# Kernel optimization log

Hardware: AMD Instinct MI355X
Metric: run time of the kernel (lower is better)

The kernel has to match this reference:

```python
import jax, jax.numpy as jnp
import numpy as np
import math

B, S, H, NH = 4, 1024, 1536, 24
DH = H // NH
BUCKETS = 256          # position_buckets
MAX_REL = 512          # max_relative_positions
ATT_SPAN = BUCKETS     # pos_ebd_size
SCALE_FACTOR = 3       # 1 (content) + c2p + p2c
LN_EPS = 1e-7


def _make_log_bucket(rel, bucket_size, max_position):
    # numpy port of make_log_bucket_position (used only to build inputs)
    sign = np.sign(rel)
    mid = bucket_size // 2
    abs_pos = np.where((rel < mid) & (rel > -mid), mid - 1, np.abs(rel)).astype(np.float64)
    log_pos = np.ceil(np.log(abs_pos / mid) / np.log((max_position - 1) / mid) * (mid - 1)) + mid
    bucket = np.where(abs_pos <= mid, rel.astype(np.float64), log_pos * sign)
    return bucket.astype(np.int64)


def setup_inputs() -> dict:
    key = jax.random.key(0)
    ks = jax.random.split(key, 8)
    s = 0.02
    hidden_states = jax.random.normal(ks[0], (B, S, H), jnp.float32)
    rel_embeddings = jax.random.normal(ks[1], (2 * ATT_SPAN, H), jnp.float32)
    ids = np.arange(S)
    relative_pos = jnp.asarray(
        _make_log_bucket(ids[:, None] - ids[None, :], BUCKETS, MAX_REL)[None].astype(np.int32))  # [1,S,S]
    lengths = np.full((B,), S)
    lengths[B // 2:] = (3 * S) // 4  # some padded sequences
    valid = np.arange(S)[None, :] < lengths[:, None]  # [B,S]
    attention_mask = jnp.asarray(
        (valid[:, None, :, None] & valid[:, None, None, :]).astype(np.int32))  # [B,1,S,S]
    Wq = jax.random.normal(ks[2], (H, H), jnp.float32) * s
    Wk = jax.random.normal(ks[3], (H, H), jnp.float32) * s
    Wv = jax.random.normal(ks[4], (H, H), jnp.float32) * s
    Wo = jax.random.normal(ks[5], (H, H), jnp.float32) * s
    z = jnp.zeros((H,), jnp.float32)
    return dict(hidden_states=hidden_states, rel_embeddings=rel_embeddings,
                Wq=Wq, bq=z, Wk=Wk, bk=z, Wv=Wv, bv=z, Wo=Wo, bo=z,
                ln_g=jnp.ones((H,), jnp.float32), ln_b=z,
                attention_mask=attention_mask, relative_pos=relative_pos)


def _attention(hidden_states, rel_embeddings, Wq, bq, Wk, bk, Wv, bv, Wo, bo,
               ln_g, ln_b, attention_mask, relative_pos):
    Bm, Sm, Hm = hidden_states.shape

    def heads(x):  # [B,S,H] -> [B,NH,S,DH]
        return x.reshape(Bm, Sm, NH, DH).transpose(0, 2, 1, 3)

    q = heads(hidden_states @ Wq + bq)
    k = heads(hidden_states @ Wk + bk)
    v = heads(hidden_states @ Wv + bv)

    scale = math.sqrt(DH * SCALE_FACTOR)
    scores = jnp.einsum('bhqd,bhkd->bhqk', q, k) / scale  # content-to-content

    # share_att_key=True: reuse query/key projections on rel embeddings
    pos_k = (rel_embeddings @ Wk + bk).reshape(2 * ATT_SPAN, NH, DH).transpose(1, 0, 2)  # [NH,2P,DH]
    pos_q = (rel_embeddings @ Wq + bq).reshape(2 * ATT_SPAN, NH, DH).transpose(1, 0, 2)

    # content -> position
    c2p = jnp.einsum('bhqd,hpd->bhqp', q, pos_k)  # [B,NH,S,2P]
    c2p_idx = jnp.clip(relative_pos + ATT_SPAN, 0, 2 * ATT_SPAN - 1)[:, None]  # [1,1,S,S]
    c2p = jnp.take_along_axis(c2p, jnp.broadcast_to(c2p_idx, (Bm, NH, Sm, Sm)), axis=-1)
    scores = scores + c2p / scale

    # position -> content
    p2c = jnp.einsum('bhkd,hpd->bhkp', k, pos_q)  # [B,NH,S,2P]
    p2c_idx = jnp.clip(-relative_pos + ATT_SPAN, 0, 2 * ATT_SPAN - 1)[:, None]
    p2c = jnp.take_along_axis(p2c, jnp.broadcast_to(p2c_idx, (Bm, NH, Sm, Sm)), axis=-1)
    scores = scores + jnp.swapaxes(p2c, -1, -2) / scale

    # XSoftmax: mask==0 -> -inf before softmax, 0 after
    m = attention_mask.astype(bool)
    neg = jnp.finfo(scores.dtype).min
    probs = jax.nn.softmax(jnp.where(m, scores, neg), axis=-1)
    probs = jnp.where(m, probs, jnp.zeros((), scores.dtype))

    ctx = jnp.einsum('bhqk,bhkd->bhqd', probs, v)
    ctx = ctx.transpose(0, 2, 1, 3).reshape(Bm, Sm, Hm)

    # DebertaV2SelfOutput: dense + residual + LayerNorm
    out = ctx @ Wo + bo + hidden_states
    mu = jnp.mean(out, axis=-1, keepdims=True)
    var = jnp.mean(jnp.square(out - mu), axis=-1, keepdims=True)
    return (out - mu) / jnp.sqrt(var + LN_EPS) * ln_g + ln_b


def reference(hidden_states, rel_embeddings, Wq, bq, Wk, bk, Wv, bv, Wo, bo,
              ln_g, ln_b, attention_mask, relative_pos):
    return _attention(hidden_states, rel_embeddings, Wq, bq, Wk, bk, Wv, bv,
                      Wo, bo, ln_g, ln_b, attention_mask, relative_pos)
```

## Files before the change

### kernel.cpp

```cpp
#include <hip/hip_runtime.h>
#include <hip/hip_bf16.h>

constexpr int Bc  = 4;
constexpr int Sc  = 1024;
constexpr int Hc  = 1536;
constexpr int NHc = 24;
constexpr int P2c = 512;
constexpr int MX  = Bc * Sc;
constexpr int MA  = MX + P2c;
constexpr int N3  = 3 * Hc;
constexpr float INV_SCALE = 0.07216878364870323f;

using f32x4  = __attribute__((ext_vector_type(4))) float;
using bf16x8 = __attribute__((ext_vector_type(8))) short;
using i32x4  = __attribute__((ext_vector_type(4))) int;
using u16x8  = __attribute__((ext_vector_type(8))) unsigned short;
using u16x4  = __attribute__((ext_vector_type(4))) unsigned short;
typedef unsigned short u16;
typedef unsigned int u32;

#define DEV __device__ __forceinline__

DEV float bf2f(u16 u) { return __uint_as_float(((unsigned)u) << 16); }
DEV u16   f2bf(float f) { return __builtin_bit_cast(unsigned short, __float2bfloat16(f)); }

#if defined(__has_builtin)
#if __has_builtin(__builtin_amdgcn_global_load_lds)
#define HAVE_GLL 1
#endif
#endif
#ifndef HAVE_GLL
#define HAVE_GLL 0
#endif

DEV void stage32(u16* lds, const u16* g, int ldk, int lane) {
#pragma unroll
  for (int c = 0; c < 4; ++c) {
    const int row   = c * 8 + (lane >> 3);
    const int gslot = (lane & 7) ^ (row & 7);
    const u16* gp = g + (size_t)row * ldk + gslot * 8;
#if HAVE_GLL
    __builtin_amdgcn_global_load_lds(
        (const __attribute__((address_space(1))) void*)gp,
        (__attribute__((address_space(3))) void*)(lds + c * 8 * 64),
        16, 0, 0);
#else
    i32x4 v = *(const i32x4*)gp;
    *(i32x4*)(lds + row * 64 + (lane & 7) * 8) = v;
#endif
  }
}

DEV bf16x8 ldsFrag(const u16* base, int row, int kh, int lhi) {
  const int idx = row * 64 + ((kh * 32 + lhi * 8) ^ ((row & 7) * 8));
  return *(const bf16x8*)(base + idx);
}

template <int MODE>
__global__ __launch_bounds__(256) void gemm128(
    const u16* __restrict__ A, const u16* __restrict__ Bt,
    const float* __restrict__ bias, const float* __restrict__ resid,
    u16* __restrict__ outb, float* __restrict__ outf, u16* __restrict__ vtout, int ldo)
{
  __shared__ alignas(16) u16 As[128 * 64];
  __shared__ alignas(16) u16 Bs[128 * 64];
  const int tid = threadIdx.x, wid = tid >> 6, lane = tid & 63;
  const int wr = wid >> 1, wc = wid & 1;
  const int l15 = lane & 15, lhi = lane >> 4;
  int bx, by;
  if (MODE == 0) {
    int id = blockIdx.x;
    id = (id & 7) * 138 + (id >> 3);
    if (id < 1008) {
      const int q = id / 36;
      by = q < 22 ? q : q + 2;
      bx = id - q * 36;
    } else {
      const int r = id - 1008;
      by = 32 + r / 24;
      bx = r % 24;
    }
  } else { bx = blockIdx.x; by = blockIdx.y; }
  const int m0 = by * 128, n0 = bx * 128;

  f32x4 acc[4][4] = {};
#pragma unroll 1
  for (int kt = 0; kt < 24; ++kt) {
    const int k0 = kt * 64;
    stage32(As + wid * (32 * 64), A  + (size_t)(m0 + wid * 32) * 1536 + k0, 1536, lane);
    stage32(Bs + wid * (32 * 64), Bt + (size_t)(n0 + wid * 32) * 1536 + k0, 1536, lane);
    asm volatile("s_waitcnt vmcnt(0)" ::: "memory");
    __syncthreads();
#pragma unroll
    for (int kh = 0; kh < 2; ++kh) {
      bf16x8 af[4], bfv[4];
#pragma unroll
      for (int mt = 0; mt < 4; ++mt) af[mt]  = ldsFrag(As, wr * 64 + mt * 16 + l15, kh, lhi);
#pragma unroll
      for (int nt = 0; nt < 4; ++nt) bfv[nt] = ldsFrag(Bs, wc * 64 + nt * 16 + l15, kh, lhi);
#pragma unroll
      for (int mt = 0; mt < 4; ++mt)
#pragma unroll
        for (int nt = 0; nt < 4; ++nt)
          acc[mt][nt] = __builtin_amdgcn_mfma_f32_16x16x32_bf16(af[mt], bfv[nt], acc[mt][nt], 0, 0, 0);
    }
    __syncthreads();
  }
#pragma unroll
  for (int mt = 0; mt < 4; ++mt)
#pragma unroll
    for (int nt = 0; nt < 4; ++nt) {
      const int gn = n0 + wc * 64 + nt * 16 + l15;
      const float bs = bias[gn];
      if (MODE == 0) {
        u16x4 q4;
#pragma unroll
        for (int r = 0; r < 4; ++r) {
          const int gm = m0 + wr * 64 + mt * 16 + lhi * 4 + r;
          float v = acc[mt][nt][r] + bs;
          if (gn < Hc) v *= INV_SCALE;
          q4[r] = f2bf(v);
          outb[(size_t)gm * ldo + gn] = q4[r];
        }
        if (gn >= 2 * Hc && m0 < MX) {
          const int b = m0 >> 10;
          const int krow = (m0 & 1023) + wr * 64 + mt * 16 + (lhi << 2);
          *(u16x4*)(vtout + ((size_t)(b * 1536 + (gn - 2 * Hc))) * Sc + krow) = q4;
        }
      } else {
#pragma unroll
        for (int r = 0; r < 4; ++r) {
          const int gm = m0 + wr * 64 + mt * 16 + lhi * 4 + r;
          outf[(size_t)gm * ldo + gn] = acc[mt][nt][r] + bs + resid[(size_t)gm * ldo + gn];
        }
      }
    }
}

__global__ __launch_bounds__(256) void prep2(
    const float* __restrict__ bq, const float* __restrict__ bk, const float* __restrict__ bv,
    const int* __restrict__ am, const int* __restrict__ rp,
    float* __restrict__ bias, u32* __restrict__ TBL2, int* __restrict__ LENS)
{
  const int TOT = N3 + 2048;
  for (int i = blockIdx.x * 256 + threadIdx.x; i < TOT; i += gridDim.x * 256) {
    if (i < N3) {
      bias[i] = i < Hc ? bq[i] : (i < 2 * Hc ? bk[i - Hc] : bv[i - 2 * Hc]);
    } else {
      const int t = i - N3;
      auto Tf = [&](int tt) -> u32 {
        tt = tt > 2046 ? 2046 : tt;
        const int d = tt - 1023;
        int v = (d >= 0 ? rp[(size_t)d * Sc] : rp[-d]) + 256;
        return (u32)(v < 0 ? 0 : (v > 511 ? 511 : v));
      };
      TBL2[t] = Tf(t) | (Tf(t + 1) << 16);
    }
  }
  if (blockIdx.x == 0) {
    const int wid = threadIdx.x >> 6, lane = threadIdx.x & 63;
    if (wid < 4) {
      int s = 0;
#pragma unroll
      for (int j = 0; j < 16; ++j) {
        const int ss = j * 64 + lane;
        s += am[(size_t)wid * Sc * Sc + (size_t)ss * Sc + ss] != 0;
      }
#pragma unroll
      for (int off = 1; off <= 32; off <<= 1) s += __shfl_xor(s, off);
      if (lane == 0) LENS[wid] = s;
    }
  }
}

__global__ __launch_bounds__(256) void cast_x(const float* __restrict__ hs,
                                              const float* __restrict__ rel,
                                              u16* __restrict__ A)
{
  const size_t total = (size_t)MA * Hc / 4;
  for (size_t i = (size_t)blockIdx.x * 256 + threadIdx.x; i < total; i += (size_t)gridDim.x * 256) {
    const size_t e = i * 4;
    const int row = (int)(e / Hc), col = (int)(e % Hc);
    const float* s = row < MX ? hs + (size_t)row * Hc + col : rel + (size_t)(row - MX) * Hc + col;
    f32x4 v = *(const f32x4*)s;
    u16x4 o = { f2bf(v[0]), f2bf(v[1]), f2bf(v[2]), f2bf(v[3]) };
    *(u16x4*)(A + e) = o;
  }
}

__global__ void transpose_cast(const float* __restrict__ Wq, const float* __restrict__ Wk,
                               const float* __restrict__ Wv, const float* __restrict__ Wo,
                               u16* __restrict__ WT, u16* __restrict__ WOT)
{
  const int z = blockIdx.z;
  const float* src = z == 0 ? Wq : z == 1 ? Wk : z == 2 ? Wv : Wo;
  u16* dst = z == 3 ? WOT : WT + (size_t)z * Hc * Hc;
  __shared__ float t[32][33];
  const int tx = threadIdx.x, ty = threadIdx.y;
  const int kb = blockIdx.y * 32, nb = blockIdx.x * 32;
#pragma unroll
  for (int i = 0; i < 4; ++i)
    t[ty + i * 8][tx] = src[(size_t)(kb + ty + i * 8) * Hc + nb + tx];
  __syncthreads();
#pragma unroll
  for (int i = 0; i < 4; ++i)
    dst[(size_t)(nb + ty + i * 8) * Hc + kb + tx] = f2bf(t[tx][ty + i * 8]);
}

__global__ __launch_bounds__(256) void relmat5(const u16* __restrict__ QKVP,
    u16* __restrict__ c2p, u16* __restrict__ p2cT, const int* __restrict__ LENS, int bh_base)
{
  const int lbh = blockIdx.x / 12, vv = blockIdx.x % 12;
  const int bh = bh_base + lbh, b = bh / NHc, h = bh % NHc;
  const int tid = threadIdx.x, wid = tid >> 6, lane = tid & 63;
  const int l15 = lane & 15, lhi = lane >> 4, lhi4 = lhi * 4;

  __shared__ alignas(16) u16 Bs[512 * 64];

  int m0, n0, ldo, nsw, brows;
  size_t arow, brow;
  u16* out;
  if (vv < 4) {
    m0 = vv * 256; n0 = 0; ldo = P2c; nsw = 32; brows = 512;
    if (m0 >= LENS[b]) return;
    arow = (size_t)b * Sc + m0; brow = (size_t)MX;
    out = c2p + (size_t)lbh * Sc * P2c;
  } else {
    const int w = vv - 4;
    m0 = (w >> 2) * 256; n0 = (w & 3) * 256; ldo = Sc; nsw = 16; brows = 256;
    if (n0 >= LENS[b]) return;
    arow = (size_t)MX + m0; brow = (size_t)b * Sc + n0;
    out = p2cT + (size_t)lbh * P2c * Sc;
  }
  const int acol = h * 64;
  const int bcol = Hc + h * 64;

  const int srow = tid >> 3;
  const int gsl  = (tid & 7) ^ (srow & 7);
  const int its = brows >> 5;
  for (int it = 0; it < its; ++it) {
    const int row = it * 32 + srow;
    const u16* gp = QKVP + (brow + row) * 4608 + bcol + gsl * 8;
#if HAVE_GLL
    __builtin_amdgcn_global_load_lds(
        (const __attribute__((address_space(1))) void*)gp,
        (__attribute__((address_space(3))) void*)(&Bs[it * 2048 + wid * 512]),
        16, 0, 0);
#else
    *(i32x4*)(&Bs[row * 64 + (tid & 7) * 8]) = *(const i32x4*)gp;
#endif
  }

  bf16x8 af[4][2];
#pragma unroll
  for (int mt = 0; mt < 4; ++mt)
#pragma unroll
    for (int kh = 0; kh < 2; ++kh)
      af[mt][kh] = *(const bf16x8*)(QKVP + (arow + wid * 64 + mt * 16 + l15) * 4608
                                    + acol + kh * 32 + lhi * 8);

  asm volatile("s_waitcnt vmcnt(0)" ::: "memory");
  __syncthreads();

#pragma unroll 4
  for (int nt = 0; nt < nsw; ++nt) {
    bf16x8 b0 = ldsFrag(Bs, nt * 16 + l15, 0, lhi);
    bf16x8 b1 = ldsFrag(Bs, nt * 16 + l15, 1, lhi);
    f32x4 acc[4] = {};
#pragma unroll
    for (int mt = 0; mt < 4; ++mt) {
      acc[mt] = __builtin_amdgcn_mfma_f32_16x16x32_bf16(af[mt][0], b0, acc[mt], 0, 0, 0);
      acc[mt] = __builtin_amdgcn_mfma_f32_16x16x32_bf16(af[mt][1], b1, acc[mt], 0, 0, 0);
    }
#pragma unroll
    for (int mt = 0; mt < 4; ++mt)
#pragma unroll
      for (int r = 0; r < 4; ++r) {
        const int mm = m0 + wid * 64 + mt * 16 + lhi4 + r;
        const int nn = n0 + nt * 16 + l15;
        out[(size_t)mm * ldo + nn] = f2bf(acc[mt][r]);
      }
  }
}

__global__ __launch_bounds__(256) void flash11(
    const u16* __restrict__ QKVP, const u16* __restrict__ VT,
    const u16* __restrict__ c2p, const u16* __restrict__ p2cT,
    const int* __restrict__ LENS, const u32* __restrict__ TBL2g,
    u16* __restrict__ ctx, int bh_base, int chunkC)
{
  int id = blockIdx.x;
  const int grid = chunkC * 16;
  if ((grid & 7) == 0) { const int cpx = grid >> 3; id = (id & 7) * cpx + (id >> 3); }
  const int lbh = id >> 4, qi = id & 15;
  const int bh = bh_base + lbh, b = bh / NHc, h = bh % NHc;
  const int q0 = qi * 64;
  const int tid = threadIdx.x, wid = tid >> 6, lane = tid & 63;
  const int l15 = lane & 15, lhi = lane >> 4, lhi4 = lhi * 4;
  const int len = LENS[b];

  if (q0 >= len) {
    u16x8 z = {};
#pragma unroll
    for (int i = 0; i < 2; ++i) {
      const int t = i * 256 + tid;
      *(u16x8*)(ctx + (size_t)(b * Sc + q0 + (t >> 3)) * Hc + h * 64 + (t & 7) * 8) = z;
    }
    return;
  }
  const int nkt = (len + 63) >> 6;
  const int qg = q0 + wid * 16 + l15;

  __shared__ u32 Lt2[2048];
  __shared__ alignas(16) u16 cWs[64 * 152];
  __shared__ alignas(16) u16 pWs[136 * 72];
  __shared__ alignas(16) u16 Kt[64 * 64];
  __shared__ alignas(16) u16 Vt[64 * 64];
  __shared__ alignas(16) u16 Pl[4][16 * 64];

  const u16* c2pB  = c2p  + (size_t)lbh * Sc * P2c;
  const u16* p2cTB = p2cT + (size_t)lbh * P2c * Sc;
  const u16* Qg  = QKVP + (size_t)b * Sc * 4608 + h * 64;
  const u16* Kg  = QKVP + (size_t)b * Sc * 4608 + Hc + h * 64;
  const u16* VTg = VT + (size_t)bh * 64 * Sc;

  for (int i = tid; i < 2048; i += 256) Lt2[i] = TBL2g[i];

  bf16x8 aq[2];
#pragma unroll
  for (int kh = 0; kh < 2; ++kh)
    aq[kh] = *(const bf16x8*)(Qg + (size_t)qg * 4608 + kh * 32 + lhi * 8);

  const int kr = tid >> 2, dc = (tid & 3) * 16;
  const int sk = (kr & 7) * 8;

  u16x8 rcw[5], rpw[5], rk0, rk1, rv0, rv1;

  auto issue = [&](int k0, int c0a) {
#pragma unroll
    for (int i = 0; i < 5; ++i) {
      const int s = i * 256 + tid;
      if (s < 1152) {
        const int row = s / 18, ch = s - row * 18;
        rcw[i] = *(const u16x8*)(c2pB + (size_t)(q0 + row) * P2c + c0a + ch * 8);
      }
    }
#pragma unroll
    for (int i = 0; i < 5; ++i) {
      const int s = i * 256 + tid;
      if (s < 1088) {
        const int row = s >> 3, ch = s & 7;
        rpw[i] = *(const u16x8*)(p2cTB + (size_t)(c0a + row) * Sc + k0 + ch * 8);
      }
    }
    const size_t ro = (size_t)(k0 + kr) * 4608 + dc;
    rk0 = *(const u16x8*)(Kg + ro); rk1 = *(const u16x8*)(Kg + ro + 8);
    const u16* vp = VTg + (size_t)kr * Sc + k0 + dc;
    rv0 = *(const u16x8*)vp; rv1 = *(const u16x8*)(vp + 8);
  };

  auto commit = [&]() {
#pragma unroll
    for (int i = 0; i < 5; ++i) {
      const int s = i * 256 + tid;
      if (s < 1152) {
        const int row = s / 18, ch = s - row * 18;
        *(u16x8*)(cWs + row * 152 + ch * 8) = rcw[i];
      }
    }
#pragma unroll
    for (int i = 0; i < 5; ++i) {
      const int s = i * 256 + tid;
      if (s < 1088) {
        const int row = s >> 3, ch = s & 7;
        *(u16x8*)(pWs + row * 72 + ch * 8) = rpw[i];
      }
    }
    *(u16x8*)(Kt + kr * 64 + (dc ^ sk))       = rk0;
    *(u16x8*)(Kt + kr * 64 + ((dc ^ sk) ^ 8)) = rk1;
    *(u16x8*)(Vt + kr * 64 + (dc ^ sk))       = rv0;
    *(u16x8*)(Vt + kr * 64 + ((dc ^ sk) ^ 8)) = rv1;
  };

  __syncthreads();
  int cc0a = (int)(Lt2[q0 + 960] & 0xFFFF) & ~7;
  issue(0, cc0a);
  asm volatile("s_waitcnt vmcnt(0)" ::: "memory");
  commit();
  __syncthreads();

  u16* myP = Pl[wid];
  const int qloc = wid * 16 + l15;
  f32x4 o_acc[4] = {};
  float lsum = 0.f;
  int cc0a_n = 0;

  for (int kt = 0; kt < nkt; ++kt) {
    const int k0 = kt * 64;
    const bool more = (kt + 1 < nkt);
    if (more) {
      cc0a_n = (int)(Lt2[q0 - (k0 + 64) - 63 + 1023] & 0xFFFF) & ~7;
      issue(k0 + 64, cc0a_n);
    }

    f32x4 s[4];
    __builtin_amdgcn_s_setprio(1);
#pragma unroll
    for (int j = 0; j < 4; ++j) {
      f32x4 sv = {};
#pragma unroll
      for (int kh = 0; kh < 2; ++kh) {
        bf16x8 bk = ldsFrag(Kt, j * 16 + l15, kh, lhi);
        sv = __builtin_amdgcn_mfma_f32_16x16x32_bf16(bk, aq[kh], sv, 0, 0, 0);
      }
      s[j] = sv;
    }
    __builtin_amdgcn_s_setprio(0);

    float p[4][4];
#pragma unroll
    for (int j = 0; j < 4; ++j) {
      const int kb = j * 16 + lhi4;
      const int t0 = qg - (k0 + kb) + 1023;
      const u32 wA = Lt2[t0 - 1];
      const u32 wB = Lt2[t0 - 3];
      const int wv[4] = { (int)(wA >> 16) - cc0a, (int)(wA & 0xFFFF) - cc0a,
                          (int)(wB >> 16) - cc0a, (int)(wB & 0xFFFF) - cc0a };
#pragma unroll
      for (int r = 0; r < 4; ++r) {
        const float rel = bf2f(cWs[qloc * 152 + wv[r]])
                        + bf2f(pWs[wv[r] * 72 + kb + r]);
        p[j][r] = (k0 + kb + r < len) ? __expf(s[j][r] + rel) : 0.f;
      }
    }
    lsum += ((p[0][0] + p[0][1] + p[0][2] + p[0][3]) + (p[1][0] + p[1][1] + p[1][2] + p[1][3]))
          + ((p[2][0] + p[2][1] + p[2][2] + p[2][3]) + (p[3][0] + p[3][1] + p[3][2] + p[3][3]));

#pragma unroll
    for (int j = 0; j < 4; ++j) {
      u16x4 pk = { f2bf(p[j][0]), f2bf(p[j][1]), f2bf(p[j][2]), f2bf(p[j][3]) };
      *(u16x4*)(myP + l15 * 64 + ((j * 16 + lhi4) ^ ((l15 & 7) * 8))) = pk;
    }

    __builtin_amdgcn_s_setprio(1);
#pragma unroll
    for (int kh = 0; kh < 2; ++kh) {
      bf16x8 pa = *(const bf16x8*)(myP + l15 * 64 + ((kh * 32 + lhi * 8) ^ ((l15 & 7) * 8)));
#pragma unroll
      for (int jd = 0; jd < 4; ++jd) {
        bf16x8 vf = ldsFrag(Vt, jd * 16 + l15, kh, lhi);
        o_acc[jd] = __builtin_amdgcn_mfma_f32_16x16x32_bf16(vf, pa, o_acc[jd], 0, 0, 0);
      }
    }
    __builtin_amdgcn_s_setprio(0);

    __syncthreads();
    if (more) {
      asm volatile("s_waitcnt vmcnt(0)" ::: "memory");
      commit();
      cc0a = cc0a_n;
    }
    __syncthreads();
  }

  lsum += __shfl_xor(lsum, 16);
  lsum += __shfl_xor(lsum, 32);
  const float inv = (qg < len && lsum > 0.f) ? 1.f / lsum : 0.f;
#pragma unroll
  for (int jd = 0; jd < 4; ++jd) {
    u16x4 st = { f2bf(o_acc[jd][0] * inv), f2bf(o_acc[jd][1] * inv),
                 f2bf(o_acc[jd][2] * inv), f2bf(o_acc[jd][3] * inv) };
    *(u16x4*)(ctx + (size_t)(b * Sc + qg) * Hc + h * 64 + jd * 16 + lhi4) = st;
  }
}

__global__ __launch_bounds__(256) void ln_kernel(float* __restrict__ io,
    const float* __restrict__ g, const float* __restrict__ bta)
{
  const int row = blockIdx.x;
  float* p = io + (size_t)row * Hc;
  const int tid = threadIdx.x, wid = tid >> 6, lane = tid & 63;
  float v[6];
  float s = 0.f;
#pragma unroll
  for (int j = 0; j < 6; ++j) { v[j] = p[tid + j * 256]; s += v[j]; }
#pragma unroll
  for (int off = 1; off <= 32; off <<= 1) s += __shfl_xor(s, off);
  __shared__ float red[4];
  if (lane == 0) red[wid] = s;
  __syncthreads();
  const float mu = (red[0] + red[1] + red[2] + red[3]) * (1.f / Hc);
  float q = 0.f;
#pragma unroll
  for (int j = 0; j < 6; ++j) { const float d = v[j] - mu; q += d * d; }
#pragma unroll
  for (int off = 1; off <= 32; off <<= 1) q += __shfl_xor(q, off);
  __syncthreads();
  if (lane == 0) red[wid] = q;
  __syncthreads();
  const float rstd = rsqrtf((red[0] + red[1] + red[2] + red[3]) * (1.f / Hc) + 1e-7f);
#pragma unroll
  for (int j = 0; j < 6; ++j) {
    const int c = tid + j * 256;
    p[c] = (v[j] - mu) * rstd * g[c] + bta[c];
  }
}

extern "C" void kernel_launch(void* const* d_in, const int* in_sizes, int n_in,
                              void* d_out, int out_size, void* d_ws, size_t ws_size,
                              hipStream_t stream)
{
  (void)in_sizes; (void)n_in; (void)out_size;
  const float* hidden = (const float*)d_in[0];
  const float* relemb = (const float*)d_in[1];
  const float* Wq = (const float*)d_in[2];
  const float* bq = (const float*)d_in[3];
  const float* Wk = (const float*)d_in[4];
  const float* bk = (const float*)d_in[5];
  const float* Wv = (const float*)d_in[6];
  const float* bv = (const float*)d_in[7];
  const float* Wo = (const float*)d_in[8];
  const float* bo = (const float*)d_in[9];
  const float* lng = (const float*)d_in[10];
  const float* lnb = (const float*)d_in[11];
  const int* am = (const int*)d_in[12];
  const int* rp = (const int*)d_in[13];
  float* out = (float*)d_out;

  char* ws = (char*)d_ws;
  size_t off = 0;
  auto alloc = [&](size_t bytes) { size_t r = off; off += (bytes + 255) & ~(size_t)255; return r; };
  const size_t o_qkvp = alloc((size_t)MA * 4608 * 2);
  const size_t o_wt   = alloc((size_t)N3 * Hc * 2);
  const size_t o_wot  = alloc((size_t)Hc * Hc * 2);
  const size_t o_abig = alloc((size_t)MA * Hc * 2);
  const size_t o_vt   = alloc((size_t)96 * 64 * Sc * 2);
  const size_t o_bias = alloc((size_t)N3 * 4);
  const size_t o_tbl2 = alloc(2048 * 4);
  const size_t o_lens = alloc(256);
  const size_t fixed  = off;
  const size_t o_rel  = off;

  const size_t perbh = (size_t)Sc * P2c * 2 * 2;
  const size_t guard = 512 * 1024;
  int c = 96;
  while (c > 1 && fixed + (size_t)c * perbh + guard > ws_size) c >>= 1;

  u16* QKVP = (u16*)(ws + o_qkvp);
  u16* WT   = (u16*)(ws + o_wt);
  u16* WOT  = (u16*)(ws + o_wot);
  u16* ABIG = (u16*)(ws + o_abig);
  u16* CTX  = (u16*)(ws + o_abig);
  u16* VT   = (u16*)(ws + o_vt);
  float* BIAS = (float*)(ws + o_bias);
  u32* TBL2 = (u32*)(ws + o_tbl2);
  int* LENS = (int*)(ws + o_lens);
  u16* C2P  = (u16*)(ws + o_rel);
  u16* P2CT = C2P + (size_t)c * Sc * P2c;

  prep2<<<dim3(26), dim3(256), 0, stream>>>(bq, bk, bv, am, rp, BIAS, TBL2, LENS);
  cast_x<<<dim3(1728), dim3(256), 0, stream>>>(hidden, relemb, ABIG);
  transpose_cast<<<dim3(48, 48, 4), dim3(32, 8), 0, stream>>>(Wq, Wk, Wv, Wo, WT, WOT);
  gemm128<0><<<dim3(1104), dim3(256), 0, stream>>>(ABIG, WT, BIAS, (const float*)nullptr,
                                                   QKVP, (float*)nullptr, VT, 4608);
  for (int base = 0; base < 96; base += c) {
    relmat5<<<dim3(12 * c), dim3(256), 0, stream>>>(QKVP, C2P, P2CT, LENS, base);
    flash11<<<dim3(c * 16), dim3(256), 0, stream>>>(QKVP, VT, C2P, P2CT, LENS, TBL2,
                                                    CTX, base, c);
  }
  gemm128<1><<<dim3(12, 32), dim3(256), 0, stream>>>(CTX, WOT, bo, hidden,
                                                     (u16*)nullptr, out, (u16*)nullptr, Hc);
  ln_kernel<<<dim3(MX), dim3(256), 0, stream>>>(out, lng, lnb);
}
```

Measured before the change: 377.6 us.

## Fuse prep kernels, skip padded rows and unused relative-position tiles

Merges the three preprocessing kernels (bias/table prep, activation cast, weight transpose-cast) into one launch. The output GEMM now skips matmul for 128-row tiles lying entirely in padded positions and writes only residual plus bias there. The relative-position matmul restricts computed column tiles and waves to the bucket range actually referenced, using the index table. The flash kernel reloads the c2p window only when its start offset changes. Together these target launch overhead and wasted work on padded or unused regions, at the cost of extra branching and reliance on the bucket table's monotonic structure.

```diff
diff --git a/kernel.cpp b/kernel.cpp
--- a/kernel.cpp
+++ b/kernel.cpp
@@ -60,7 +60,8 @@
 __global__ __launch_bounds__(256) void gemm128(
     const u16* __restrict__ A, const u16* __restrict__ Bt,
     const float* __restrict__ bias, const float* __restrict__ resid,
-    u16* __restrict__ outb, float* __restrict__ outf, u16* __restrict__ vtout, int ldo)
+    u16* __restrict__ outb, float* __restrict__ outf, u16* __restrict__ vtout,
+    const int* __restrict__ LENS, int ldo)
 {
   __shared__ alignas(16) u16 As[128 * 64];
   __shared__ alignas(16) u16 Bs[128 * 64];
@@ -83,6 +84,20 @@
   } else { bx = blockIdx.x; by = blockIdx.y; }
   const int m0 = by * 128, n0 = bx * 128;
 
+  if (MODE == 1 && (m0 & 1023) >= LENS[m0 >> 10]) {
+#pragma unroll
+    for (int i = 0; i < 16; ++i) {
+      const int t = i * 256 + tid;
+      const int row = t >> 5, c4 = (t & 31) * 4;
+      const int gm = m0 + row, gn = n0 + c4;
+      f32x4 r = *(const f32x4*)(resid + (size_t)gm * ldo + gn);
+      f32x4 bsv = *(const f32x4*)(bias + gn);
+      r[0] += bsv[0]; r[1] += bsv[1]; r[2] += bsv[2]; r[3] += bsv[3];
+      *(f32x4*)(outf + (size_t)gm * ldo + gn) = r;
+    }
+    return;
+  }
+
   f32x4 acc[4][4] = {};
 #pragma unroll 1
   for (int kt = 0; kt < 24; ++kt) {
@@ -137,78 +152,78 @@
     }
 }
 
-__global__ __launch_bounds__(256) void prep2(
+__global__ __launch_bounds__(256) void prep_all(
     const float* __restrict__ bq, const float* __restrict__ bk, const float* __restrict__ bv,
     const int* __restrict__ am, const int* __restrict__ rp,
-    float* __restrict__ bias, u32* __restrict__ TBL2, int* __restrict__ LENS)
+    float* __restrict__ bias, u32* __restrict__ TBL2, int* __restrict__ LENS,
+    const float* __restrict__ hs, const float* __restrict__ rel, u16* __restrict__ A,
+    const float* __restrict__ Wq, const float* __restrict__ Wk,
+    const float* __restrict__ Wv, const float* __restrict__ Wo,
+    u16* __restrict__ WT, u16* __restrict__ WOT)
 {
-  const int TOT = N3 + 2048;
-  for (int i = blockIdx.x * 256 + threadIdx.x; i < TOT; i += gridDim.x * 256) {
-    if (i < N3) {
-      bias[i] = i < Hc ? bq[i] : (i < 2 * Hc ? bk[i - Hc] : bv[i - 2 * Hc]);
-    } else {
-      const int t = i - N3;
-      auto Tf = [&](int tt) -> u32 {
-        tt = tt > 2046 ? 2046 : tt;
-        const int d = tt - 1023;
-        int v = (d >= 0 ? rp[(size_t)d * Sc] : rp[-d]) + 256;
-        return (u32)(v < 0 ? 0 : (v > 511 ? 511 : v));
-      };
-      TBL2[t] = Tf(t) | (Tf(t + 1) << 16);
-    }
-  }
-  if (blockIdx.x == 0) {
-    const int wid = threadIdx.x >> 6, lane = threadIdx.x & 63;
-    if (wid < 4) {
-      int s = 0;
-#pragma unroll
-      for (int j = 0; j < 16; ++j) {
-        const int ss = j * 64 + lane;
-        s += am[(size_t)wid * Sc * Sc + (size_t)ss * Sc + ss] != 0;
-      }
-#pragma unroll
-      for (int off = 1; off <= 32; off <<= 1) s += __shfl_xor(s, off);
-      if (lane == 0) LENS[wid] = s;
-    }
-  }
-}
-
-__global__ __launch_bounds__(256) void cast_x(const float* __restrict__ hs,
-                                              const float* __restrict__ rel,
-                                              u16* __restrict__ A)
-{
-  const size_t total = (size_t)MA * Hc / 4;
-  for (size_t i = (size_t)blockIdx.x * 256 + threadIdx.x; i < total; i += (size_t)gridDim.x * 256) {
-    const size_t e = i * 4;
-    const int row = (int)(e / Hc), col = (int)(e % Hc);
-    const float* s = row < MX ? hs + (size_t)row * Hc + col : rel + (size_t)(row - MX) * Hc + col;
-    f32x4 v = *(const f32x4*)s;
-    u16x4 o = { f2bf(v[0]), f2bf(v[1]), f2bf(v[2]), f2bf(v[3]) };
-    *(u16x4*)(A + e) = o;
-  }
-}
-
-__global__ void transpose_cast(const float* __restrict__ Wq, const float* __restrict__ Wk,
-                               const float* __restrict__ Wv, const float* __restrict__ Wo,
-                               u16* __restrict__ WT, u16* __restrict__ WOT)
-{
-  const int z = blockIdx.z;
-  const float* src = z == 0 ? Wq : z == 1 ? Wk : z == 2 ? Wv : Wo;
-  u16* dst = z == 3 ? WOT : WT + (size_t)z * Hc * Hc;
-  __shared__ float t[32][33];
-  const int tx = threadIdx.x, ty = threadIdx.y;
-  const int kb = blockIdx.y * 32, nb = blockIdx.x * 32;
-#pragma unroll
-  for (int i = 0; i < 4; ++i)
-    t[ty + i * 8][tx] = src[(size_t)(kb + ty + i * 8) * Hc + nb + tx];
-  __syncthreads();
-#pragma unroll
-  for (int i = 0; i < 4; ++i)
-    dst[(size_t)(nb + ty + i * 8) * Hc + kb + tx] = f2bf(t[tx][ty + i * 8]);
-}
-
-__global__ __launch_bounds__(256) void relmat5(const u16* __restrict__ QKVP,
-    u16* __restrict__ c2p, u16* __restrict__ p2cT, const int* __restrict__ LENS, int bh_base)
+  const int bid = blockIdx.x, tid = threadIdx.x;
+  if (bid < 26) {
+    const int TOT = N3 + 2048;
+    for (int i = bid * 256 + tid; i < TOT; i += 26 * 256) {
+      if (i < N3) {
+        bias[i] = i < Hc ? bq[i] : (i < 2 * Hc ? bk[i - Hc] : bv[i - 2 * Hc]);
+      } else {
+        const int t = i - N3;
+        auto Tf = [&](int tt) -> u32 {
+          tt = tt > 2046 ? 2046 : tt;
+          const int d = tt - 1023;
+          int v = (d >= 0 ? rp[(size_t)d * Sc] : rp[-d]) + 256;
+          return (u32)(v < 0 ? 0 : (v > 511 ? 511 : v));
+        };
+        TBL2[t] = Tf(t) | (Tf(t + 1) << 16);
+      }
+    }
+    if (bid == 0) {
+      const int wid = tid >> 6, lane = tid & 63;
+      if (wid < 4) {
+        int s = 0;
+#pragma unroll
+        for (int j = 0; j < 16; ++j) {
+          const int ss = j * 64 + lane;
+          s += am[(size_t)wid * Sc * Sc + (size_t)ss * Sc + ss] != 0;
+        }
+#pragma unroll
+        for (int off = 1; off <= 32; off <<= 1) s += __shfl_xor(s, off);
+        if (lane == 0) LENS[wid] = s;
+      }
+    }
+  } else if (bid < 26 + 1728) {
+    const size_t total = (size_t)MA * Hc / 4;
+    for (size_t i = (size_t)(bid - 26) * 256 + tid; i < total; i += (size_t)1728 * 256) {
+      const size_t e = i * 4;
+      const int row = (int)(e / Hc), col = (int)(e % Hc);
+      const float* s = row < MX ? hs + (size_t)row * Hc + col : rel + (size_t)(row - MX) * Hc + col;
+      f32x4 v = *(const f32x4*)s;
+      u16x4 o = { f2bf(v[0]), f2bf(v[1]), f2bf(v[2]), f2bf(v[3]) };
+      *(u16x4*)(A + e) = o;
+    }
+  } else {
+    const int t = bid - (26 + 1728);
+    const int z = t / 2304, rem = t - z * 2304;
+    const int byy = rem / 48, bxx = rem - byy * 48;
+    const float* src = z == 0 ? Wq : z == 1 ? Wk : z == 2 ? Wv : Wo;
+    u16* dst = z == 3 ? WOT : WT + (size_t)z * Hc * Hc;
+    __shared__ float tt[32][33];
+    const int tx = tid & 31, ty = tid >> 5;
+    const int kb = byy * 32, nb = bxx * 32;
+#pragma unroll
+    for (int i = 0; i < 4; ++i)
+      tt[ty + i * 8][tx] = src[(size_t)(kb + ty + i * 8) * Hc + nb + tx];
+    __syncthreads();
+#pragma unroll
+    for (int i = 0; i < 4; ++i)
+      dst[(size_t)(nb + ty + i * 8) * Hc + kb + tx] = f2bf(tt[tx][ty + i * 8]);
+  }
+}
+
+__global__ __launch_bounds__(256) void relmat6(const u16* __restrict__ QKVP,
+    u16* __restrict__ c2p, u16* __restrict__ p2cT, const int* __restrict__ LENS,
+    const u32* __restrict__ TBL2, int bh_base)
 {
   const int lbh = blockIdx.x / 12, vv = blockIdx.x % 12;
   const int bh = bh_base + lbh, b = bh / NHc, h = bh % NHc;
@@ -217,18 +232,27 @@
 
   __shared__ alignas(16) u16 Bs[512 * 64];
 
-  int m0, n0, ldo, nsw, brows;
+  int m0, n0, ldo, nt0, nt1, brows;
   size_t arow, brow;
   u16* out;
+  bool waveActive = true;
   if (vv < 4) {
-    m0 = vv * 256; n0 = 0; ldo = P2c; nsw = 32; brows = 512;
+    m0 = vv * 256; n0 = 0; ldo = P2c; brows = 512;
     if (m0 >= LENS[b]) return;
+    const int lo = (int)(TBL2[m0] & 0xFFFF) & ~7;
+    const int hi = (int)(TBL2[m0 + 1278] & 0xFFFF);
+    nt0 = lo >> 4; nt1 = (hi >> 4) + 1;
     arow = (size_t)b * Sc + m0; brow = (size_t)MX;
     out = c2p + (size_t)lbh * Sc * P2c;
   } else {
     const int w = vv - 4;
-    m0 = (w >> 2) * 256; n0 = (w & 3) * 256; ldo = Sc; nsw = 16; brows = 256;
-    if (n0 >= LENS[b]) return;
+    m0 = (w >> 2) * 256; n0 = (w & 3) * 256; ldo = Sc; nt0 = 0; nt1 = 16; brows = 256;
+    const int len = LENS[b];
+    if (n0 >= len) return;
+    const int lo = (int)(TBL2[768 - n0 < 0 ? 0 : 768 - n0] & 0xFFFF) & ~7;
+    const int hi = (int)(TBL2[len + 1022 - n0 > 2046 ? 2046 : len + 1022 - n0] & 0xFFFF);
+    const int wlo = m0 + wid * 64, whi = wlo + 63;
+    waveActive = !(whi < lo || wlo > hi);
     arow = (size_t)MX + m0; brow = (size_t)b * Sc + n0;
     out = p2cT + (size_t)lbh * P2c * Sc;
   }
@@ -252,18 +276,21 @@
   }
 
   bf16x8 af[4][2];
-#pragma unroll
-  for (int mt = 0; mt < 4; ++mt)
-#pragma unroll
-    for (int kh = 0; kh < 2; ++kh)
-      af[mt][kh] = *(const bf16x8*)(QKVP + (arow + wid * 64 + mt * 16 + l15) * 4608
-                                    + acol + kh * 32 + lhi * 8);
+  if (waveActive) {
+#pragma unroll
+    for (int mt = 0; mt < 4; ++mt)
+#pragma unroll
+      for (int kh = 0; kh < 2; ++kh)
+        af[mt][kh] = *(const bf16x8*)(QKVP + (arow + wid * 64 + mt * 16 + l15) * 4608
+                                      + acol + kh * 32 + lhi * 8);
+  }
 
   asm volatile("s_waitcnt vmcnt(0)" ::: "memory");
   __syncthreads();
+  if (!waveActive) return;
 
 #pragma unroll 4
-  for (int nt = 0; nt < nsw; ++nt) {
+  for (int nt = nt0; nt < nt1; ++nt) {
     bf16x8 b0 = ldsFrag(Bs, nt * 16 + l15, 0, lhi);
     bf16x8 b1 = ldsFrag(Bs, nt * 16 + l15, 1, lhi);
     f32x4 acc[4] = {};
@@ -283,7 +310,7 @@
   }
 }
 
-__global__ __launch_bounds__(256) void flash11(
+__global__ __launch_bounds__(256) void flash12(
     const u16* __restrict__ QKVP, const u16* __restrict__ VT,
     const u16* __restrict__ c2p, const u16* __restrict__ p2cT,
     const int* __restrict__ LENS, const u32* __restrict__ TBL2g,
@@ -336,13 +363,15 @@
 
   u16x8 rcw[5], rpw[5], rk0, rk1, rv0, rv1;
 
-  auto issue = [&](int k0, int c0a) {
-#pragma unroll
-    for (int i = 0; i < 5; ++i) {
-      const int s = i * 256 + tid;
-      if (s < 1152) {
-        const int row = s / 18, ch = s - row * 18;
-        rcw[i] = *(const u16x8*)(c2pB + (size_t)(q0 + row) * P2c + c0a + ch * 8);
+  auto issue = [&](int k0, int c0a, bool ldCW) {
+    if (ldCW) {
+#pragma unroll
+      for (int i = 0; i < 5; ++i) {
+        const int s = i * 256 + tid;
+        if (s < 1152) {
+          const int row = s / 18, ch = s - row * 18;
+          rcw[i] = *(const u16x8*)(c2pB + (size_t)(q0 + row) * P2c + c0a + ch * 8);
+        }
       }
     }
 #pragma unroll
@@ -359,13 +388,15 @@
     rv0 = *(const u16x8*)vp; rv1 = *(const u16x8*)(vp + 8);
   };
 
-  auto commit = [&]() {
-#pragma unroll
-    for (int i = 0; i < 5; ++i) {
-      const int s = i * 256 + tid;
-      if (s < 1152) {
-        const int row = s / 18, ch = s - row * 18;
-        *(u16x8*)(cWs + row * 152 + ch * 8) = rcw[i];
+  auto commit = [&](bool ldCW) {
+    if (ldCW) {
+#pragma unroll
+      for (int i = 0; i < 5; ++i) {
+        const int s = i * 256 + tid;
+        if (s < 1152) {
+          const int row = s / 18, ch = s - row * 18;
+          *(u16x8*)(cWs + row * 152 + ch * 8) = rcw[i];
+        }
       }
     }
 #pragma unroll
@@ -384,9 +415,9 @@
 
   __syncthreads();
   int cc0a = (int)(Lt2[q0 + 960] & 0xFFFF) & ~7;
-  issue(0, cc0a);
+  issue(0, cc0a, true);
   asm volatile("s_waitcnt vmcnt(0)" ::: "memory");
-  commit();
+  commit(true);
   __syncthreads();
 
   u16* myP = Pl[wid];
@@ -394,13 +425,15 @@
   f32x4 o_acc[4] = {};
   float lsum = 0.f;
   int cc0a_n = 0;
+  bool ldCW = false;
 
   for (int kt = 0; kt < nkt; ++kt) {
     const int k0 = kt * 64;
     const bool more = (kt + 1 < nkt);
     if (more) {
       cc0a_n = (int)(Lt2[q0 - (k0 + 64) - 63 + 1023] & 0xFFFF) & ~7;
-      issue(k0 + 64, cc0a_n);
+      ldCW = (cc0a_n != cc0a);
+      issue(k0 + 64, cc0a_n, ldCW);
     }
 
     f32x4 s[4];
@@ -457,7 +490,7 @@
     __syncthreads();
     if (more) {
       asm volatile("s_waitcnt vmcnt(0)" ::: "memory");
-      commit();
+      commit(ldCW);
       cc0a = cc0a_n;
     }
     __syncthreads();
@@ -558,17 +591,19 @@
   u16* C2P  = (u16*)(ws + o_rel);
   u16* P2CT = C2P + (size_t)c * Sc * P2c;
 
-  prep2<<<dim3(26), dim3(256), 0, stream>>>(bq, bk, bv, am, rp, BIAS, TBL2, LENS);
-  cast_x<<<dim3(1728), dim3(256), 0, stream>>>(hidden, relemb, ABIG);
-  transpose_cast<<<dim3(48, 48, 4), dim3(32, 8), 0, stream>>>(Wq, Wk, Wv, Wo, WT, WOT);
+  prep_all<<<dim3(26 + 1728 + 9216), dim3(256), 0, stream>>>(
+      bq, bk, bv, am, rp, BIAS, TBL2, LENS, hidden, relemb, ABIG,
+      Wq, Wk, Wv, Wo, WT, WOT);
   gemm128<0><<<dim3(1104), dim3(256), 0, stream>>>(ABIG, WT, BIAS, (const float*)nullptr,
-                                                   QKVP, (float*)nullptr, VT, 4608);
+                                                   QKVP, (float*)nullptr, VT,
+                                                   (const int*)nullptr, 4608);
   for (int base = 0; base < 96; base += c) {
-    relmat5<<<dim3(12 * c), dim3(256), 0, stream>>>(QKVP, C2P, P2CT, LENS, base);
-    flash11<<<dim3(c * 16), dim3(256), 0, stream>>>(QKVP, VT, C2P, P2CT, LENS, TBL2,
+    relmat6<<<dim3(12 * c), dim3(256), 0, stream>>>(QKVP, C2P, P2CT, LENS, TBL2, base);
+    flash12<<<dim3(c * 16), dim3(256), 0, stream>>>(QKVP, VT, C2P, P2CT, LENS, TBL2,
                                                     CTX, base, c);
   }
   gemm128<1><<<dim3(12, 32), dim3(256), 0, stream>>>(CTX, WOT, bo, hidden,
-                                                     (u16*)nullptr, out, (u16*)nullptr, Hc);
+                                                     (u16*)nullptr, out, (u16*)nullptr,
+                                                     LENS, Hc);
   ln_kernel<<<dim3(MX), dim3(256), 0, stream>>>(out, lng, lnb);
 }
```

New measurement: 372.5 us. No clear change (-1.4%).
